# Optimization experiments

Measured on AMD Instinct MI355X. Metric: run time of the kernel, lower is better.

## Reference

```python
import jax, jax.numpy as jnp
import numpy as np
from jax import lax

NS = 262144          # number of forcing samples (len(TA))
DT = 60              # model time step (s)
DT_FORCING = 3600    # forcing time step (s)


def setup_inputs() -> dict:
    key = jax.random.key(0)
    k1, k2 = jax.random.split(key)
    pk = jnp.zeros((2,), dtype=jnp.float32) - 10.0  # exp(pk): K0 ~ 1/(rho*H), K1 ~ damping r
    TAr = 0.1 * jax.random.normal(k1, (NS,), dtype=jnp.float32)  # wind stress, zonal
    TAi = 0.1 * jax.random.normal(k2, (NS,), dtype=jnp.float32)  # wind stress, meridional
    fc = jnp.float32(1e-4)   # Coriolis frequency
    U0 = jnp.float32(0.0)
    V0 = jnp.float32(0.0)
    return {"pk": pk, "TAr": TAr, "TAi": TAi, "fc": fc, "U0": U0, "V0": V0,
            "dt": DT, "dt_forcing": DT_FORCING}


def reference(pk, TAr, TAi, fc, U0, V0, dt, dt_forcing):
    # Faithful slab model: per outer step `it` (0..ns-1), nsub inner Euler steps of
    #   U <- U + dt*(-i*fc*U + K0*TA_interp - K1*U)
    # starting from U[:, it-1] (or the initial condition for it==0).
    # Since the update is affine linear, each inner loop collapses exactly to
    #   U_next = a^nsub * U_old + dt*K0 * sum_j a^(nsub-1-j) * TA_interp[it, j]
    # with a = 1 + dt*(-i*fc - K1), which we then scan over the ns outer steps.
    nsub = int(dt_forcing) // int(dt)
    ns = TAr.shape[0]
    TA = TAr + 1j * TAi                                # complex64, (ns,)
    K = jnp.exp(pk)                                    # K_transform('exp')
    K0, K1 = K[0], K[1]
    a = 1.0 + dt * (-1j * fc - K1)                     # complex64 scalar

    # time interpolation of forcing, exactly as in the source:
    # itm = it*nsub + j ; itf = it // nsub ; aa = (itm mod nsub)/nsub = j/nsub
    it = jnp.arange(ns)
    itf = it // nsub                                   # NOTE: it//nsub, as in original
    itsup = jnp.where(itf + 1 >= ns, -1, itf)
    aa = (jnp.arange(nsub).astype(jnp.float32)) / nsub  # (nsub,)
    TA_int = ((1.0 - aa)[None, :] * TA[itf - 1][:, None]
              + aa[None, :] * TA[itsup][:, None])       # (ns, nsub) complex64

    # inner-loop closed form
    w = a ** (nsub - 1 - jnp.arange(nsub))              # (nsub,) complex64
    b = (dt * K0) * (TA_int @ w)                        # (ns,) complex64
    A = a ** nsub

    u_init = (U0 + 1j * V0).astype(TA.dtype)

    def step(u, bt):
        u = A * u + bt
        return u, u

    _, Useq = lax.scan(step, u_init, b)                 # (ns,)
    U = Useq[None, :]                                   # (nl=1, ns)
    return jnp.real(U), jnp.imag(U)
```

## Files before the change

kernel.cpp:

```cpp
#include <hip/hip_runtime.h>

#define BLK  256
#define OPT  4
#define HIST 6
#define BR   48
#define TMAX 64

struct c32 { float x, y; };
__device__ __forceinline__ c32 mkc(float x, float y) { c32 r; r.x = x; r.y = y; return r; }
__device__ __forceinline__ c32 cmul(c32 a, c32 b) {
    return mkc(a.x * b.x - a.y * b.y, a.x * b.y + a.y * b.x);
}
__device__ __forceinline__ c32 cfma(c32 a, c32 u, c32 b) {
    return mkc(fmaf(a.x, u.x, fmaf(-a.y, u.y, b.x)),
               fmaf(a.x, u.y, fmaf( a.y, u.x, b.y)));
}
__device__ __forceinline__ c32 cpow(c32 base, unsigned e, int nbits) {
    c32 res = mkc(1.0f, 0.0f); c32 p = base;
    for (int b = 0; b < nbits; ++b) {
        if (e & (1u << b)) res = cmul(res, p);
        p = cmul(p, p);
    }
    return res;
}

__global__ __launch_bounds__(BLK) void slab_runs_kernel(
    const float* __restrict__ pk,
    const float* __restrict__ TAr,
    const float* __restrict__ TAi,
    const float* __restrict__ fcp,
    const float* __restrict__ U0p,
    const float* __restrict__ V0p,
    const int*   __restrict__ dtp,
    const int*   __restrict__ dtfp,
    float*       __restrict__ out,
    int ns)
{
    __shared__ float2 sApow[TMAX];
    __shared__ float2 sGr[TMAX];
    __shared__ float2 sB[BR];

    const int t = threadIdx.x;
    const float K0 = expf(pk[0]);
    const float K1 = expf(pk[1]);
    const float fc = fcp[0];
    const int   dti  = dtp[0];
    const float dt   = (float)dti;
    const int   nsub = dtfp[0] / dti;

    const int base = blockIdx.x * (BLK * OPT);
    const unsigned m_first = (unsigned)base / (unsigned)nsub;
    const int run_base = (int)m_first - HIST;
    const int nrun_total = (ns + nsub - 1) / nsub;

    if (t < 64) {
        const c32 a = mkc(1.0f - dt * K1, -dt * fc);
        c32 pa = cpow(a, (unsigned)t, 6);
        const float dn = (float)nsub;
        float c1 = (t < nsub) ? (float)(t + 1) / dn        : 0.0f;
        float c2 = (t < nsub) ? (float)(nsub - 1 - t) / dn : 0.0f;
        float s1x = c1 * pa.x, s1y = c1 * pa.y;
        float s2x = c2 * pa.x, s2y = c2 * pa.y;
        #pragma unroll
        for (int off = 32; off >= 1; off >>= 1) {
            s1x += __shfl_xor(s1x, off, 64);
            s1y += __shfl_xor(s1y, off, 64);
            s2x += __shfl_xor(s2x, off, 64);
            s2y += __shfl_xor(s2y, off, 64);
        }
        const float sc = dt * K0;
        const c32 Cp = mkc(sc * s1x, sc * s1y);
        const c32 Cc = mkc(sc * s2x, sc * s2y);

        const c32 Ao = cpow(a, (unsigned)nsub, 7);

        if (t < nsub && t < TMAX) {
            c32 ap = cpow(Ao, (unsigned)(t + 1), 7);
            sApow[t] = make_float2(ap.x, ap.y);
            c32 om = mkc(1.0f - Ao.x, -Ao.y);
            float d = om.x * om.x + om.y * om.y;
            c32 inv = mkc(om.x / d, -om.y / d);
            c32 g = cmul(mkc(1.0f - ap.x, -ap.y), inv);
            sGr[t] = make_float2(g.x, g.y);
        }
        if (t < BR) {
            int k = run_base + t;
            float bx = 0.0f, by = 0.0f;
            if (k >= 0 && k < nrun_total) {
                int prev = k - 1; if (prev < 0) prev += ns;
                int cur  = (k + 1 >= ns) ? (ns - 1) : k;
                c32 tp = mkc(TAr[prev], TAi[prev]);
                c32 tc = mkc(TAr[cur],  TAi[cur]);
                c32 b1 = cmul(Cp, tp);
                c32 b2 = cmul(Cc, tc);
                bx = b1.x + b2.x; by = b1.y + b2.y;
            }
            sB[t] = make_float2(bx, by);
        }
    }
    __syncthreads();

    const int i0 = base + t * OPT;
    if (i0 < ns) {
        const unsigned m = (unsigned)i0 / (unsigned)nsub;
        const int r  = i0 - (int)m * nsub;
        const int lm = (int)m - run_base;

        float2 f;
        f = sApow[nsub - 1]; const c32 Ablk = mkc(f.x, f.y);
        f = sGr[nsub - 1];   const c32 g59  = mkc(f.x, f.y);
        f = sApow[0];        const c32 Aout = mkc(f.x, f.y);

        f = sB[lm - HIST]; c32 S = mkc(f.x, f.y);
        #pragma unroll
        for (int j = HIST - 1; j >= 1; --j) {
            f = sB[lm - j];
            S = cfma(Ablk, S, mkc(f.x, f.y));
        }
        c32 uprev = cmul(g59, S);

        c32 apm = mkc(1.0f, 0.0f);
        #pragma unroll
        for (int j = 0; j < HIST; ++j) {
            c32 tt = cmul(apm, Ablk);
            bool mlt = (j < (int)m);
            apm.x = mlt ? tt.x : apm.x;
            apm.y = mlt ? tt.y : apm.y;
        }
        if ((int)m <= HIST) {
            c32 u0 = mkc(U0p[0], V0p[0]);
            uprev = cfma(apm, u0, uprev);
        }

        f = sB[lm];     const c32 bm  = mkc(f.x, f.y);
        f = sB[lm + 1]; const c32 bm1 = mkc(f.x, f.y);
        f = sApow[r];   const c32 Ar  = mkc(f.x, f.y);
        f = sGr[r];     const c32 gr  = mkc(f.x, f.y);

        c32 t1 = cmul(Ar, uprev);
        c32 t2 = cmul(bm, gr);
        c32 U  = mkc(t1.x + t2.x, t1.y + t2.y);

        float ur[OPT], ui[OPT];
        ur[0] = U.x; ui[0] = U.y;
        #pragma unroll
        for (int k = 1; k < OPT; ++k) {
            int rk = r + k;
            c32 bb = (rk < nsub) ? bm : bm1;
            U = cfma(Aout, U, bb);
            ur[k] = U.x; ui[k] = U.y;
        }

        if (((ns & 3) == 0) && (i0 + OPT <= ns)) {
            *(float4*)(out + i0)      = make_float4(ur[0], ur[1], ur[2], ur[3]);
            *(float4*)(out + ns + i0) = make_float4(ui[0], ui[1], ui[2], ui[3]);
        } else {
            for (int k = 0; k < OPT; ++k) {
                if (i0 + k < ns) {
                    out[i0 + k]      = ur[k];
                    out[ns + i0 + k] = ui[k];
                }
            }
        }
    }
}

extern "C" void kernel_launch(void* const* d_in, const int* in_sizes, int n_in,
                              void* d_out, int out_size, void* d_ws, size_t ws_size,
                              hipStream_t stream) {
    const float* pk  = (const float*)d_in[0];
    const float* TAr = (const float*)d_in[1];
    const float* TAi = (const float*)d_in[2];
    const float* fc  = (const float*)d_in[3];
    const float* U0  = (const float*)d_in[4];
    const float* V0  = (const float*)d_in[5];
    const int*   dt  = (const int*)d_in[6];
    const int*   dtf = (const int*)d_in[7];

    int ns = in_sizes[1];
    int blocks = (ns + BLK * OPT - 1) / (BLK * OPT);
    slab_runs_kernel<<<blocks, BLK, 0, stream>>>(pk, TAr, TAi, fc, U0, V0, dt, dtf,
                                                 (float*)d_out, ns);
}
```

Baseline: 11.54 us.

## Compute constants redundantly per thread and stage raw forcing in shared memory

Moves the setup work (powers of a, the interpolation weight sums, the block factor and the g terms) out of a single-wave serial prologue and has every thread compute them redundantly in registers. Shared memory now holds only the raw forcing values, loaded in parallel by 192 threads, and the b coefficients and per-thread A^r and g_r terms are rebuilt on the fly. cpow becomes a branchless, unrolled template. This shortens the serial latency chain before the barrier, at the cost of extra per-thread ALU work and extra shared-memory reads.

Measured after the change: 11.22 us. -2.8%, faster.

```diff
diff --git a/kernel.cpp b/kernel.cpp
--- a/kernel.cpp
+++ b/kernel.cpp
@@ -4,7 +4,6 @@
 #define OPT  4
 #define HIST 6
 #define BR   48
-#define TMAX 64
 
 struct c32 { float x, y; };
 __device__ __forceinline__ c32 mkc(float x, float y) { c32 r; r.x = x; r.y = y; return r; }
@@ -15,10 +14,15 @@
     return mkc(fmaf(a.x, u.x, fmaf(-a.y, u.y, b.x)),
                fmaf(a.x, u.y, fmaf( a.y, u.x, b.y)));
 }
-__device__ __forceinline__ c32 cpow(c32 base, unsigned e, int nbits) {
+template <int NB>
+__device__ __forceinline__ c32 cpow(c32 base, unsigned e) {
     c32 res = mkc(1.0f, 0.0f); c32 p = base;
-    for (int b = 0; b < nbits; ++b) {
-        if (e & (1u << b)) res = cmul(res, p);
+    #pragma unroll
+    for (int b = 0; b < NB; ++b) {
+        bool on = (e >> b) & 1u;
+        c32 t = cmul(res, p);
+        res.x = on ? t.x : res.x;
+        res.y = on ? t.y : res.y;
         p = cmul(p, p);
     }
     return res;
@@ -36,68 +40,67 @@
     float*       __restrict__ out,
     int ns)
 {
-    __shared__ float2 sApow[TMAX];
-    __shared__ float2 sGr[TMAX];
-    __shared__ float2 sB[BR];
+    __shared__ float sRaw[4][BR];
 
     const int t = threadIdx.x;
-    const float K0 = expf(pk[0]);
-    const float K1 = expf(pk[1]);
-    const float fc = fcp[0];
-    const int   dti  = dtp[0];
+    const int base = blockIdx.x * (BLK * OPT);
+
+    const float pk0 = pk[0], pk1 = pk[1];
+    const float fc  = fcp[0];
+    const float u0r = U0p[0], u0i = V0p[0];
+    const int   dti = dtp[0];
+    const int   dtf = dtfp[0];
+
+    const int   nsub = dtf / dti;
     const float dt   = (float)dti;
-    const int   nsub = dtfp[0] / dti;
 
-    const int base = blockIdx.x * (BLK * OPT);
-    const unsigned m_first = (unsigned)base / (unsigned)nsub;
-    const int run_base = (int)m_first - HIST;
-    const int nrun_total = (ns + nsub - 1) / nsub;
+    const int   nrun_total = (ns + nsub - 1) / nsub;
+    const int   run_base   = base / nsub - HIST;
 
-    if (t < 64) {
-        const c32 a = mkc(1.0f - dt * K1, -dt * fc);
-        c32 pa = cpow(a, (unsigned)t, 6);
-        const float dn = (float)nsub;
-        float c1 = (t < nsub) ? (float)(t + 1) / dn        : 0.0f;
-        float c2 = (t < nsub) ? (float)(nsub - 1 - t) / dn : 0.0f;
-        float s1x = c1 * pa.x, s1y = c1 * pa.y;
-        float s2x = c2 * pa.x, s2y = c2 * pa.y;
-        #pragma unroll
-        for (int off = 32; off >= 1; off >>= 1) {
-            s1x += __shfl_xor(s1x, off, 64);
-            s1y += __shfl_xor(s1y, off, 64);
-            s2x += __shfl_xor(s2x, off, 64);
-            s2y += __shfl_xor(s2y, off, 64);
+    if (t < 4 * BR) {
+        const int q = t / BR;
+        const int j = t - q * BR;
+        const int k = run_base + j;
+        float v = 0.0f;
+        if (k >= 0 && k < nrun_total) {
+            int prev = k - 1; if (prev < 0) prev += ns;
+            int cur  = (k + 1 >= ns) ? (ns - 1) : k;
+            const float* src = (q == 0) ? TAr : (q == 1) ? TAi : (q == 2) ? TAr : TAi;
+            v = src[(q < 2) ? prev : cur];
         }
-        const float sc = dt * K0;
-        const c32 Cp = mkc(sc * s1x, sc * s1y);
-        const c32 Cc = mkc(sc * s2x, sc * s2y);
+        sRaw[q][j] = v;
+    }
 
-        const c32 Ao = cpow(a, (unsigned)nsub, 7);
+    const float K0 = expf(pk0);
+    const float K1 = expf(pk1);
+    const c32 a = mkc(1.0f - dt * K1, -dt * fc);
 
-        if (t < nsub && t < TMAX) {
-            c32 ap = cpow(Ao, (unsigned)(t + 1), 7);
-            sApow[t] = make_float2(ap.x, ap.y);
-            c32 om = mkc(1.0f - Ao.x, -Ao.y);
-            float d = om.x * om.x + om.y * om.y;
-            c32 inv = mkc(om.x / d, -om.y / d);
-            c32 g = cmul(mkc(1.0f - ap.x, -ap.y), inv);
-            sGr[t] = make_float2(g.x, g.y);
-        }
-        if (t < BR) {
-            int k = run_base + t;
-            float bx = 0.0f, by = 0.0f;
-            if (k >= 0 && k < nrun_total) {
-                int prev = k - 1; if (prev < 0) prev += ns;
-                int cur  = (k + 1 >= ns) ? (ns - 1) : k;
-                c32 tp = mkc(TAr[prev], TAi[prev]);
-                c32 tc = mkc(TAr[cur],  TAi[cur]);
-                c32 b1 = cmul(Cp, tp);
-                c32 b2 = cmul(Cc, tc);
-                bx = b1.x + b2.x; by = b1.y + b2.y;
-            }
-            sB[t] = make_float2(bx, by);
-        }
+    const int lane = t & 63;
+    c32 pa = cpow<6>(a, (unsigned)lane);
+    const float dn = (float)nsub;
+    float c1 = (lane < nsub) ? (float)(lane + 1) / dn        : 0.0f;
+    float c2 = (lane < nsub) ? (float)(nsub - 1 - lane) / dn : 0.0f;
+    float s1x = c1 * pa.x, s1y = c1 * pa.y;
+    float s2x = c2 * pa.x, s2y = c2 * pa.y;
+    #pragma unroll
+    for (int off = 32; off >= 1; off >>= 1) {
+        s1x += __shfl_xor(s1x, off, 64);
+        s1y += __shfl_xor(s1y, off, 64);
+        s2x += __shfl_xor(s2x, off, 64);
+        s2y += __shfl_xor(s2y, off, 64);
     }
+    const float sc = dt * K0;
+    const c32 Cp = mkc(sc * s1x, sc * s1y);
+    const c32 Cc = mkc(sc * s2x, sc * s2y);
+
+    const c32 Aout = cpow<7>(a, (unsigned)nsub);
+    const c32 Ablk = cpow<7>(Aout, (unsigned)nsub);
+
+    const c32 om = mkc(1.0f - Aout.x, -Aout.y);
+    const float dinv = 1.0f / (om.x * om.x + om.y * om.y);
+    const c32 inv1mA = mkc(om.x * dinv, -om.y * dinv);
+    const c32 g59 = cmul(mkc(1.0f - Ablk.x, -Ablk.y), inv1mA);
+
     __syncthreads();
 
     const int i0 = base + t * OPT;
@@ -106,47 +109,35 @@
         const int r  = i0 - (int)m * nsub;
         const int lm = (int)m - run_base;
 
-        float2 f;
-        f = sApow[nsub - 1]; const c32 Ablk = mkc(f.x, f.y);
-        f = sGr[nsub - 1];   const c32 g59  = mkc(f.x, f.y);
-        f = sApow[0];        const c32 Aout = mkc(f.x, f.y);
+        auto bq = [&](int q) -> c32 {
+            c32 tp = mkc(sRaw[0][q], sRaw[1][q]);
+            c32 tc = mkc(sRaw[2][q], sRaw[3][q]);
+            return cfma(Cc, tc, cmul(Cp, tp));
+        };
 
-        f = sB[lm - HIST]; c32 S = mkc(f.x, f.y);
+        c32 S = bq(lm - HIST);
         #pragma unroll
-        for (int j = HIST - 1; j >= 1; --j) {
-            f = sB[lm - j];
-            S = cfma(Ablk, S, mkc(f.x, f.y));
-        }
+        for (int j = HIST - 1; j >= 1; --j)
+            S = cfma(Ablk, S, bq(lm - j));
         c32 uprev = cmul(g59, S);
 
-        c32 apm = mkc(1.0f, 0.0f);
-        #pragma unroll
-        for (int j = 0; j < HIST; ++j) {
-            c32 tt = cmul(apm, Ablk);
-            bool mlt = (j < (int)m);
-            apm.x = mlt ? tt.x : apm.x;
-            apm.y = mlt ? tt.y : apm.y;
-        }
         if ((int)m <= HIST) {
-            c32 u0 = mkc(U0p[0], V0p[0]);
-            uprev = cfma(apm, u0, uprev);
+            c32 apm = cpow<3>(Ablk, m);
+            uprev = cfma(apm, mkc(u0r, u0i), uprev);
         }
 
-        f = sB[lm];     const c32 bm  = mkc(f.x, f.y);
-        f = sB[lm + 1]; const c32 bm1 = mkc(f.x, f.y);
-        f = sApow[r];   const c32 Ar  = mkc(f.x, f.y);
-        f = sGr[r];     const c32 gr  = mkc(f.x, f.y);
+        const c32 bm  = bq(lm);
+        const c32 bm1 = bq(lm + 1);
+        const c32 Ar  = cpow<6>(Aout, (unsigned)(r + 1));
+        const c32 gr  = cmul(mkc(1.0f - Ar.x, -Ar.y), inv1mA);
 
-        c32 t1 = cmul(Ar, uprev);
-        c32 t2 = cmul(bm, gr);
-        c32 U  = mkc(t1.x + t2.x, t1.y + t2.y);
+        c32 U = cfma(Ar, uprev, cmul(bm, gr));
 
         float ur[OPT], ui[OPT];
         ur[0] = U.x; ui[0] = U.y;
         #pragma unroll
         for (int k = 1; k < OPT; ++k) {
-            int rk = r + k;
-            c32 bb = (rk < nsub) ? bm : bm1;
+            c32 bb = (r + k < nsub) ? bm : bm1;
             U = cfma(Aout, U, bb);
             ur[k] = U.x; ui[k] = U.y;
         }
```
